# Kernel optimization log

Measured on AMD Instinct MI355X. Metric: run time of the kernel, lower is better.

Reference implementation:

```python
import jax, jax.numpy as jnp
from jax import lax
import numpy as np

HID = 128; NRAD = 32; NAZ = 8; EPS_BN = 1e-5

def _bn(x, p):
    # p: [4, C] = (gamma, beta, running_mean, running_var); eval-mode batchnorm
    g, b, m, v = p
    sh = (1, -1) + (1,) * (x.ndim - 2)
    return (x - m.reshape(sh)) * (g.reshape(sh) / jnp.sqrt(v.reshape(sh) + EPS_BN)) + b.reshape(sh)

def _conv2d(x, w, b):
    y = lax.conv_general_dilated(x, w, (1, 1), 'SAME', dimension_numbers=('NCHW', 'OIHW', 'NCHW'))
    return y + b.reshape(1, -1, 1, 1)

def _conv1d(x, w, b):
    y = lax.conv_general_dilated(x, w, (1,), 'SAME', dimension_numbers=('NCH', 'OIH', 'NCH'))
    return y + b.reshape(1, -1, 1)

def setup_inputs():
    key = jax.random.key(0)
    ks = iter(jax.random.split(key, 48))
    def W(shape, s=0.05):
        return jax.random.normal(next(ks), shape, jnp.float32) * s
    def bias(c):
        return jax.random.normal(next(ks), (c,), jnp.float32) * 0.01
    def bn(c):
        g = 1.0 + 0.1 * jax.random.normal(next(ks), (c,), jnp.float32)
        b = 0.1 * jax.random.normal(next(ks), (c,), jnp.float32)
        m = 0.05 * jax.random.normal(next(ks), (c,), jnp.float32)
        v = 0.5 + jax.random.uniform(next(ks), (c,), jnp.float32)
        return jnp.stack([g, b, m, v])
    B, C, H, Wd = 16, 3, 256, 256
    h2, h4 = HID // 2, HID // 4
    comb = h2 + h4 + h4 + NAZ * C * 2  # 64+32+32+48 = 176
    return {
        'x': jax.random.normal(next(ks), (B, C, H, Wd), jnp.float32),
        'mw1': W((h2, C, 3, 3)), 'mb1': bias(h2), 'mbn1': bn(h2),
        'mw2': W((h2, h2, 3, 3)), 'mb2': bias(h2), 'mbn2': bn(h2),
        'pw1': W((h4, C, 3, 3)), 'pb1': bias(h4), 'pbn1': bn(h4),
        'pw2': W((h4, h4, 3, 3)), 'pb2': bias(h4), 'pbn2': bn(h4),
        'rw1': W((h4, C, 3)), 'rb1': bias(h4), 'rbn1': bn(h4),
        'rw2': W((h4, h4, 3)), 'rb2': bias(h4), 'rbn2': bn(h4),
        'lw1': W((HID * 2, comb)), 'lb1': bias(HID * 2),
        'lng': jnp.ones((HID * 2,), jnp.float32), 'lnb': jnp.zeros((HID * 2,), jnp.float32),
        'lw2': W((HID, HID * 2)), 'lb2': bias(HID),
    }

def _forward(x, mw1, mb1, mbn1, mw2, mb2, mbn2, pw1, pb1, pbn1, pw2, pb2, pbn2,
             rw1, rb1, rbn1, rw2, rb2, rbn2, lw1, lb1, lng, lnb, lw2, lb2):
    B, C, H, Wd = x.shape
    xf = jnp.clip(x.astype(jnp.float32), -10.0, 10.0)
    freq = jnp.fft.rfft2(xf, axes=(-2, -1))                         # [B,C,H,W//2+1] complex
    mag = jnp.clip(jnp.abs(freq), 1e-8, 1e6)
    mag_log = jnp.clip(jnp.log1p(mag), -20.0, 20.0)
    phase = jnp.clip(jnp.angle(freq) / np.pi, -1.0, 1.0)

    # static frequency-grid bin indices
    fy = jnp.fft.fftfreq(H).astype(jnp.float32)
    fx = jnp.fft.rfftfreq(Wd).astype(jnp.float32)
    fyg, fxg = jnp.meshgrid(fy, fx, indexing='ij')
    radius = jnp.sqrt(fxg ** 2 + fyg ** 2)
    rbins = jnp.clip((radius / (radius.max() + 1e-8) * (NRAD - 1)).astype(jnp.int32), 0, NRAD - 1).reshape(-1)
    angle = jnp.arctan2(fyg, fxg + 1e-8)
    abins = jnp.clip(((angle + np.pi) / (2 * np.pi) * NAZ).astype(jnp.int32), 0, NAZ - 1).reshape(-1)

    mag_flat = mag.reshape(B, C, -1)                                # [B,C,N]
    # radial power spectrum: segment mean via one-hot contraction
    r_oh = jax.nn.one_hot(rbins, NRAD, dtype=jnp.float32)           # [N,NRAD]
    r_cnt = jnp.maximum(r_oh.sum(0), 1.0)
    radial = jnp.clip(jnp.einsum('bcn,nk->bck', mag_flat, r_oh) / r_cnt, 0.0, 1e6)  # [B,C,NRAD]

    # azimuthal mean / unbiased std per angular sector (single pass sum/sumsq/count)
    a_oh = jax.nn.one_hot(abins, NAZ, dtype=jnp.float32)            # [N,NAZ]
    a_cnt = a_oh.sum(0)
    s1 = jnp.einsum('bcn,nk->bck', mag_flat, a_oh)
    s2 = jnp.einsum('bcn,nk->bck', mag_flat ** 2, a_oh)
    a_mean = s1 / a_cnt
    a_var = (s2 - a_cnt * a_mean ** 2) / jnp.maximum(a_cnt - 1.0, 1.0)
    a_std = jnp.sqrt(jnp.maximum(a_var, 0.0))
    # torch cat order: mean_bin0, std_bin0, mean_bin1, std_bin1, ... each [B,C]
    az = jnp.stack([a_mean.transpose(0, 2, 1), a_std.transpose(0, 2, 1)], axis=2).reshape(B, NAZ * 2 * C)
    az = jnp.nan_to_num(az, nan=0.0, posinf=1e4, neginf=-1e4)

    # bilinear upsample to (H,W); jax.image.resize uses half-pixel centers == align_corners=False
    mag_sp = jax.image.resize(mag_log, (B, C, H, Wd), 'bilinear')
    ph_sp = jax.image.resize(phase, (B, C, H, Wd), 'bilinear')

    mag_feat = jax.nn.relu(_bn(_conv2d(mag_sp, mw1, mb1), mbn1))
    mag_feat = jax.nn.relu(_bn(_conv2d(mag_feat, mw2, mb2), mbn2))
    mag_pool = mag_feat.mean((2, 3))
    ph_feat = jax.nn.relu(_bn(_conv2d(ph_sp, pw1, pb1), pbn1))
    ph_feat = jax.nn.relu(_bn(_conv2d(ph_feat, pw2, pb2), pbn2))
    ph_pool = ph_feat.mean((2, 3))

    rf = jax.nn.relu(_bn(_conv1d(radial, rw1, rb1), rbn1))
    rf = jax.nn.relu(_bn(_conv1d(rf, rw2, rb2), rbn2))
    rf = rf.mean(-1)                                                # AdaptiveAvgPool1d(1)+Flatten

    comb = jnp.concatenate([mag_pool, ph_pool, rf, az], axis=1)    # [B,176]
    comb = jnp.nan_to_num(comb, nan=0.0, posinf=1e4, neginf=-1e4)
    h = comb @ lw1.T + lb1
    mu = h.mean(-1, keepdims=True)
    var = ((h - mu) ** 2).mean(-1, keepdims=True)
    h = (h - mu) / jnp.sqrt(var + 1e-5) * lng + lnb                 # LayerNorm
    h = jax.nn.relu(h)                                              # dropout = identity (eval)
    out = h @ lw2.T + lb2
    out = jnp.clip(out, -100.0, 100.0)
    return jnp.nan_to_num(out, nan=0.0, posinf=100.0, neginf=-100.0)

def reference(x, mw1, mb1, mbn1, mw2, mb2, mbn2, pw1, pb1, pbn1, pw2, pb2, pbn2,
              rw1, rb1, rbn1, rw2, rb2, rbn2, lw1, lb1, lng, lnb, lw2, lb2):
    return _forward(x, mw1, mb1, mbn1, mw2, mb2, mbn2, pw1, pb1, pbn1, pw2, pb2, pbn2,
                    rw1, rb1, rbn1, rw2, rb2, rbn2, lw1, lb1, lng, lnb, lw2, lb2)
```

## Files before the change

kernel.cpp:

```cpp
#include <hip/hip_runtime.h>
#include <math.h>

#define PI_F 3.14159274101257324f
#define TWO_PI_256 0.02454369260617026f
#define TWO_PI_16  0.39269908169872414f

typedef __attribute__((ext_vector_type(8))) short bf16x8;
typedef __attribute__((ext_vector_type(4))) float f32x4;

static const size_t OFF_FC    = 0;
static const size_t OFF_MLOG  = 3170304;
static const size_t OFF_PH    = 4755456;
static const size_t OFF_RSUM  = 9486336;
static const size_t OFF_RCNT  = OFF_RSUM + 1536;
static const size_t OFF_AS1   = OFF_RCNT + 32;
static const size_t OFF_AS2   = OFF_AS1 + 384;
static const size_t OFF_ACNT  = OFF_AS2 + 384;
static const size_t OFF_MPOOL = OFF_ACNT + 8;
static const size_t OFF_PPOOL = OFF_MPOOL + 1024;
static const size_t OFF_RF    = OFF_PPOOL + 512;
static const size_t OFF_PAR   = OFF_RF + 512;
static const size_t OFF_WBM   = OFF_PAR + 512;
static const size_t OFF_WBP   = OFF_WBM + 18432;
static const size_t OFF_W1BM  = OFF_WBP + 4608;
static const size_t OFF_W1BP  = OFF_W1BM + 1024;

__device__ __forceinline__ float fix_nan(float v, float pinf, float ninf) {
  if (isnan(v)) return 0.f;
  if (isinf(v)) return v > 0.f ? pinf : ninf;
  return v;
}

__device__ __forceinline__ unsigned short f2bf(float f) {
  unsigned u = __float_as_uint(f);
  unsigned r = (u + 0x7FFFu + ((u >> 16) & 1u)) >> 16;
  return (unsigned short)r;
}

__device__ __forceinline__ void fold_bn(const float* bn, int C, int c, float cb,
                                        float* s, float* t) {
  float g = bn[c], b = bn[C + c], m = bn[2 * C + c], v = bn[3 * C + c];
  float sc = g / sqrtf(v + 1e-5f);
  *s = sc;
  *t = b + (cb - m) * sc;
}

__global__ __launch_bounds__(256) void row_fft_prep(
    const float* __restrict__ x, float* __restrict__ Fc, float* __restrict__ zbuf,
    const float* __restrict__ mw1, const float* __restrict__ pw1,
    const float* __restrict__ mw2, const float* __restrict__ pw2,
    const float* __restrict__ mb1, const float* __restrict__ mbn1,
    const float* __restrict__ mb2, const float* __restrict__ mbn2,
    const float* __restrict__ pb1, const float* __restrict__ pbn1,
    const float* __restrict__ pb2, const float* __restrict__ pbn2,
    const float* __restrict__ rb1, const float* __restrict__ rbn1,
    const float* __restrict__ rb2, const float* __restrict__ rbn2,
    float* __restrict__ par, unsigned short* __restrict__ wbm,
    unsigned short* __restrict__ wbp, unsigned short* __restrict__ w1bm,
    unsigned short* __restrict__ w1bp) {
  const int blk = blockIdx.x;
  const int tid = threadIdx.x;
  if (blk >= 12288) {
    int idx = (blk - 12288) * 256 + tid;
    if (idx < 36864) {
      int pos = idx / 4096, rem = idx % 4096;
      int oc = rem >> 6, ci = rem & 63;
      wbm[idx] = f2bf(mw2[(oc * 64 + ci) * 9 + pos]);
    } else if (idx < 46080) {
      int i = idx - 36864;
      int pos = i / 1024, rem = i % 1024;
      int oc = rem >> 5, ci = rem & 31;
      wbp[i] = f2bf(pw2[(oc * 32 + ci) * 9 + pos]);
    } else if (idx < 46336) {
      int i = idx - 46080;
      float s, t;
      if (i < 64)       { fold_bn(mbn1, 64, i, mb1[i], &s, &t);          par[i] = s;       par[64 + i] = t; }
      else if (i < 128) { int c = i - 64;  fold_bn(mbn2, 64, c, mb2[c], &s, &t); par[128 + c] = s; par[192 + c] = t; }
      else if (i < 160) { int c = i - 128; fold_bn(pbn1, 32, c, pb1[c], &s, &t); par[256 + c] = s; par[288 + c] = t; }
      else if (i < 192) { int c = i - 160; fold_bn(pbn2, 32, c, pb2[c], &s, &t); par[320 + c] = s; par[352 + c] = t; }
      else if (i < 224) { int c = i - 192; fold_bn(rbn1, 32, c, rb1[c], &s, &t); par[384 + c] = s; par[416 + c] = t; }
      else              { int c = i - 224; fold_bn(rbn2, 32, c, rb2[c], &s, &t); par[448 + c] = s; par[480 + c] = t; }
    } else if (idx < 48384) {
      int i = idx - 46336;
      int oc = i >> 5, k = i & 31;
      w1bm[i] = (k < 27) ? f2bf(mw1[oc * 27 + k]) : (unsigned short)0;
    } else if (idx < 49408) {
      int i = idx - 48384;
      int oc = i >> 5, k = i & 31;
      w1bp[i] = (k < 27) ? f2bf(pw1[oc * 27 + k]) : (unsigned short)0;
    }
    return;
  }
  if (blk == 0) {
    for (int i = tid; i < 3880; i += 256) zbuf[i] = 0.f;
  }
  __shared__ float xr[256];
  __shared__ float2 sS[256];
  {
    float v = x[(size_t)blk * 256 + tid];
    xr[tid] = fminf(fmaxf(v, -10.f), 10.f);
  }
  __syncthreads();
  {
    int b16 = tid >> 4, m = tid & 15;
    float sW, cW;
    sincosf(TWO_PI_16 * (float)m, &sW, &cW);
    float sr = 0.f, si = 0.f, wr = 1.f, wi = 0.f;
#pragma unroll
    for (int a = 0; a < 16; ++a) {
      float xv = xr[a * 16 + b16];
      sr = fmaf(xv, wr, sr);
      si = fmaf(xv, wi, si);
      float nr = wr * cW + wi * sW;
      float ni = wi * cW - wr * sW;
      wr = nr; wi = ni;
    }
    sS[b16 * 16 + m] = make_float2(sr, si);
  }
  __syncthreads();
  if (tid < 129) {
    int m2 = tid & 15;
    float sK, cK;
    sincosf(TWO_PI_256 * (float)tid, &sK, &cK);
    float fr = 0.f, fi = 0.f, wr = 1.f, wi = 0.f;
#pragma unroll
    for (int bb = 0; bb < 16; ++bb) {
      float2 s = sS[bb * 16 + m2];
      fr = fmaf(s.x, wr, fr); fr = fmaf(-s.y, wi, fr);
      fi = fmaf(s.x, wi, fi); fi = fmaf(s.y, wr, fi);
      float nr = wr * cK + wi * sK;
      float ni = wi * cK - wr * sK;
      wr = nr; wi = ni;
    }
    float2* o = (float2*)Fc;
    o[(size_t)blk * 129 + tid] = make_float2(fr, fi);
  }
}

__global__ __launch_bounds__(256) void col_fft_stats(
    const float* __restrict__ Fc, float* __restrict__ mlog, float* __restrict__ ph,
    float* __restrict__ rsum, float* __restrict__ rcnt, float* __restrict__ as1,
    float* __restrict__ as2, float* __restrict__ acnt) {
  const int k = blockIdx.x, b = blockIdx.y;
  const int tid = threadIdx.x;
  const int cp = tid >> 7;
  __shared__ float2 col[3][256];
  __shared__ float2 sS[3][256];
  __shared__ float l_rs[3][2][32];
  __shared__ float l_rc[32];
  __shared__ float l_s1[3][2][8], l_s2[3][2][8];
  __shared__ float l_ac[8];
  for (int i = tid; i < 192; i += 256) {
    int c = i / 64, r = i % 64;
    l_rs[c][r >> 5][r & 31] = 0.f;
  }
  if (tid < 32) l_rc[tid] = 0.f;
  if (tid < 48) { int c = tid / 16, r = tid % 16; l_s1[c][r >> 3][r & 7] = 0.f; l_s2[c][r >> 3][r & 7] = 0.f; }
  if (tid < 8) l_ac[tid] = 0.f;
  const float2* fc = (const float2*)Fc;
#pragma unroll
  for (int c = 0; c < 3; ++c)
    col[c][tid] = fc[((size_t)((b * 3 + c) * 256) + tid) * 129 + k];
  __syncthreads();
  {
    int b16 = tid >> 4, m = tid & 15;
    float sW, cW;
    sincosf(TWO_PI_16 * (float)m, &sW, &cW);
#pragma unroll
    for (int c = 0; c < 3; ++c) {
      float sr = 0.f, si = 0.f, wr = 1.f, wi = 0.f;
#pragma unroll
      for (int a = 0; a < 16; ++a) {
        float2 v = col[c][a * 16 + b16];
        sr = fmaf(v.x, wr, sr); sr = fmaf(-v.y, wi, sr);
        si = fmaf(v.x, wi, si); si = fmaf(v.y, wr, si);
        float nr = wr * cW + wi * sW;
        float ni = wi * cW - wr * sW;
        wr = nr; wi = ni;
      }
      sS[c][b16 * 16 + m] = make_float2(sr, si);
    }
  }
  __syncthreads();
  const int j = tid;
  float sK, cK;
  sincosf(TWO_PI_256 * (float)j, &sK, &cK);
  float gr[3], gi[3];
#pragma unroll
  for (int c = 0; c < 3; ++c) {
    float fr = 0.f, fi = 0.f, wr = 1.f, wi = 0.f;
#pragma unroll
    for (int bb = 0; bb < 16; ++bb) {
      float2 s = sS[c][bb * 16 + (j & 15)];
      fr = fmaf(s.x, wr, fr); fr = fmaf(-s.y, wi, fr);
      fi = fmaf(s.x, wi, fi); fi = fmaf(s.y, wr, fi);
      float nr = wr * cK + wi * sK;
      float ni = wi * cK - wr * sK;
      wr = nr; wi = ni;
    }
    gr[c] = fr; gi[c] = fi;
  }
  float fy = (float)(j < 128 ? j : j - 256) * (1.0f / 256.0f);
  float fx = (float)k * (1.0f / 256.0f);
  float rad = sqrtf(fx * fx + fy * fy);
  float denom = sqrtf(0.5f) + 1e-8f;
  int rb = (int)((rad / denom) * 31.0f);
  rb = rb < 0 ? 0 : (rb > 31 ? 31 : rb);
  float ang = atan2f(fy, fx + 1e-8f);
  int ab = (int)((ang + PI_F) / (2.0f * PI_F) * 8.0f);
  ab = ab < 0 ? 0 : (ab > 7 ? 7 : ab);
#pragma unroll
  for (int c = 0; c < 3; ++c) {
    float mag = sqrtf(gr[c] * gr[c] + gi[c] * gi[c]);
    mag = fminf(fmaxf(mag, 1e-8f), 1e6f);
    float ml = fminf(fmaxf(log1pf(mag), -20.f), 20.f);
    float p = fminf(fmaxf(atan2f(gi[c], gr[c]) / PI_F, -1.f), 1.f);
    size_t oidx = ((size_t)((b * 3 + c) * 256) + j) * 129 + k;
    mlog[oidx] = ml;
    ph[oidx] = p;
    atomicAdd(&l_rs[c][cp][rb], mag);
    atomicAdd(&l_s1[c][cp][ab], mag);
    atomicAdd(&l_s2[c][cp][ab], mag * mag);
  }
  if (b == 0) {
    atomicAdd(&l_rc[rb], 1.0f);
    atomicAdd(&l_ac[ab], 1.0f);
  }
  __syncthreads();
  if (tid < 96) {
    int c = tid / 32, i2 = tid % 32;
    atomicAdd(&rsum[(b * 3 + c) * 32 + i2], l_rs[c][0][i2] + l_rs[c][1][i2]);
  } else if (tid < 120) {
    int t2 = tid - 96;
    int c = t2 / 8, a2 = t2 % 8;
    atomicAdd(&as1[(b * 3 + c) * 8 + a2], l_s1[c][0][a2] + l_s1[c][1][a2]);
    atomicAdd(&as2[(b * 3 + c) * 8 + a2], l_s2[c][0][a2] + l_s2[c][1][a2]);
  }
  if (b == 0) {
    if (tid < 32) atomicAdd(&rcnt[tid], l_rc[tid]);
    else if (tid < 40) atomicAdd(&acnt[tid - 32], l_ac[tid - 32]);
  }
}

template <int C2>
__global__ __launch_bounds__(256, (C2 == 64 ? 3 : 4)) void conv_mfma(
    const float* __restrict__ src,
    const unsigned short* __restrict__ w1b,
    const unsigned short* __restrict__ wB,
    const float* __restrict__ s1, const float* __restrict__ t1,
    const float* __restrict__ s2, const float* __restrict__ t2,
    float* __restrict__ pool) {
  constexpr int HALVES = C2 / 32;
  constexpr int ST = 40;
  constexpr int WNT = C2 / 32;

  __shared__ float s_in[3][20][20];
  __shared__ float s_sc1[C2], s_sh1[C2];
  __shared__ __align__(16) unsigned short s_f1[324 * ST];

  const int tid = threadIdx.x;
  const int b = blockIdx.z;
  const int tx0 = blockIdx.x * 16, ty0 = blockIdx.y * 16;
  const int lane = tid & 63, wv = tid >> 6;
  const int ln = lane & 15, q = lane >> 4;
  const int ntg = wv & 1, half_w = wv >> 1;
  const int ocb0 = ntg * WNT * 16;

  for (int idx = tid; idx < 1200; idx += 256) {
    int c = idx / 400, r = idx % 400, iy = r / 20, ix = r % 20;
    int gy = ty0 - 2 + iy, gx = tx0 - 2 + ix;
    float v = 0.f;
    if ((unsigned)gy < 256u && (unsigned)gx < 256u) {
      float srcx = ((float)gx + 0.5f) * (129.0f / 256.0f) - 0.5f;
      float fl = floorf(srcx);
      float w = srcx - fl;
      int x0 = (int)fl, x1 = x0 + 1;
      x0 = x0 < 0 ? 0 : x0;
      x1 = x1 > 128 ? 128 : x1;
      const float* rowp = src + ((size_t)(b * 3 + c) * 256 + gy) * 129;
      v = rowp[x0] * (1.f - w) + rowp[x1] * w;
    }
    s_in[c][iy][ix] = v;
  }
  if (tid < C2) { s_sc1[tid] = s1[tid]; s_sh1[tid] = t1[tid]; }
  __syncthreads();

  const float* sp = &s_in[0][0][0];
  int koff[8];
#pragma unroll
  for (int j = 0; j < 8; ++j) {
    int k = q * 8 + j;
    if (k < 27) {
      int c = k / 9, rr = k - c * 9, dy = rr / 3, dx = rr - dy * 3;
      koff[j] = (c * 20 + dy) * 20 + dx;
    } else koff[j] = -1;
  }

  f32x4 acc[WNT][8];
#pragma unroll
  for (int w = 0; w < WNT; ++w)
#pragma unroll
    for (int i = 0; i < 8; ++i)
      acc[w][i] = (f32x4){0.f, 0.f, 0.f, 0.f};

  const int rbase = half_w * 8;

  for (int hf = 0; hf < HALVES; ++hf) {
    if (hf > 0) __syncthreads();
    bf16x8 b1h[2];
    float c1sc[2][4], c1sh[2][4];
#pragma unroll
    for (int w = 0; w < 2; ++w) {
      int nt = hf * 2 + w;
      b1h[w] = *(const bf16x8*)&w1b[(nt * 16 + ln) * 32 + q * 8];
#pragma unroll
      for (int r = 0; r < 4; ++r) {
        c1sc[w][r] = s_sc1[hf * 32 + w * 16 + q * 4 + r];
        c1sh[w][r] = s_sh1[hf * 32 + w * 16 + q * 4 + r];
      }
    }
    for (int mt = wv; mt < 21; mt += 4) {
      int p = mt * 16 + ln;
      int pc = p < 324 ? p : 0;
      int py = pc / 18, px = pc - py * 18;
      int pix = py * 20 + px;
      union { bf16x8 v; unsigned u[4]; } af;
#pragma unroll
      for (int jj = 0; jj < 4; ++jj) {
        float v0 = (koff[2 * jj] >= 0) ? sp[koff[2 * jj] + pix] : 0.f;
        float v1 = (koff[2 * jj + 1] >= 0) ? sp[koff[2 * jj + 1] + pix] : 0.f;
        af.u[jj] = (unsigned)f2bf(v0) | ((unsigned)f2bf(v1) << 16);
      }
      bool inim = false;
      if (p < 324) {
        int gy = ty0 - 1 + py, gx = tx0 - 1 + px;
        inim = ((unsigned)gy < 256u) && ((unsigned)gx < 256u);
      }
#pragma unroll
      for (int w = 0; w < 2; ++w) {
        f32x4 c1 = __builtin_amdgcn_mfma_f32_16x16x32_bf16(
            b1h[w], af.v, (f32x4){0.f, 0.f, 0.f, 0.f}, 0, 0, 0);
        if (p < 324) {
          float v0 = inim ? fmaxf(fmaf(c1[0], c1sc[w][0], c1sh[w][0]), 0.f) : 0.f;
          float v1 = inim ? fmaxf(fmaf(c1[1], c1sc[w][1], c1sh[w][1]), 0.f) : 0.f;
          float v2 = inim ? fmaxf(fmaf(c1[2], c1sc[w][2], c1sh[w][2]), 0.f) : 0.f;
          float v3 = inim ? fmaxf(fmaf(c1[3], c1sc[w][3], c1sh[w][3]), 0.f) : 0.f;
          uint2 pk;
          pk.x = (unsigned)f2bf(v0) | ((unsigned)f2bf(v1) << 16);
          pk.y = (unsigned)f2bf(v2) | ((unsigned)f2bf(v3) << 16);
          *(uint2*)&s_f1[p * ST + w * 16 + q * 4] = pk;
        }
      }
    }
    __syncthreads();
#pragma unroll
    for (int kx = 0; kx < 3; ++kx) {
      bf16x8 Bf[WNT * 3];
#pragma unroll
      for (int w = 0; w < WNT; ++w)
#pragma unroll
        for (int ky = 0; ky < 3; ++ky)
          Bf[w * 3 + ky] = *(const bf16x8*)&wB[((size_t)(ky * 3 + kx) * C2 + ocb0 + w * 16 + ln) * C2 +
                                               hf * 32 + q * 8];
      bf16x8 a[10];
#pragma unroll
      for (int rr = 0; rr < 10; ++rr)
        a[rr] = *(const bf16x8*)&s_f1[((rbase + rr) * 18 + ln + kx) * ST + q * 8];
#pragma unroll
      for (int ky = 0; ky < 3; ++ky)
#pragma unroll
        for (int w = 0; w < WNT; ++w)
#pragma unroll
          for (int i = 0; i < 8; ++i)
            acc[w][i] = __builtin_amdgcn_mfma_f32_16x16x32_bf16(a[i + ky], Bf[w * 3 + ky],
                                                                acc[w][i], 0, 0, 0);
    }
  }

#pragma unroll
  for (int w = 0; w < WNT; ++w) {
    const int oc = ocb0 + w * 16 + ln;
    const float sc = s2[oc], sh = t2[oc];
    float v = 0.f;
#pragma unroll
    for (int i = 0; i < 8; ++i)
#pragma unroll
      for (int r = 0; r < 4; ++r)
        v += fmaxf(fmaf(acc[w][i][r], sc, sh), 0.f);
    v += __shfl_xor(v, 16);
    v += __shfl_xor(v, 32);
    if (q == 0) atomicAdd(&pool[b * C2 + oc], v);
  }
}

__global__ __launch_bounds__(256) void final_mlp(
    const float* __restrict__ rsum, const float* __restrict__ rcnt,
    const float* __restrict__ rw1, const float* __restrict__ rw2,
    const float* __restrict__ sr1, const float* __restrict__ tr1,
    const float* __restrict__ sr2, const float* __restrict__ tr2,
    const float* __restrict__ mpool, const float* __restrict__ ppool,
    const float* __restrict__ as1, const float* __restrict__ as2,
    const float* __restrict__ acnt,
    const float* __restrict__ lw1, const float* __restrict__ lb1,
    const float* __restrict__ lng, const float* __restrict__ lnb,
    const float* __restrict__ lw2, const float* __restrict__ lb2,
    float* __restrict__ out) {
  int b = blockIdx.x, t = threadIdx.x;
  __shared__ float rad[3][32];
  __shared__ float rf1[32][32];
  __shared__ float rf2[32][32];
  __shared__ float rfv[32];
  __shared__ float comb[176];
  __shared__ float red[256];
  __shared__ float hrelu[256];
  __shared__ float s_mu, s_var;

  if (t < 96) {
    int c = t / 32, i = t % 32;
    float cnt = fmaxf(rcnt[i], 1.0f);
    float v = rsum[(b * 3 + c) * 32 + i] / cnt;
    rad[c][i] = fminf(fmaxf(v, 0.f), 1e6f);
  }
  __syncthreads();
  for (int idx = t; idx < 1024; idx += 256) {
    int oc = idx >> 5, i = idx & 31;
    float a = 0.f;
    for (int c = 0; c < 3; ++c)
#pragma unroll
      for (int d = 0; d < 3; ++d) {
        int ii = i + d - 1;
        if (ii >= 0 && ii < 32) a = fmaf(rad[c][ii], rw1[(oc * 3 + c) * 3 + d], a);
      }
    rf1[oc][i] = fmaxf(fmaf(a, sr1[oc], tr1[oc]), 0.f);
  }
  __syncthreads();
  for (int idx = t; idx < 1024; idx += 256) {
    int oc = idx >> 5, i = idx & 31;
    float a = 0.f;
    for (int c = 0; c < 32; ++c)
#pragma unroll
      for (int d = 0; d < 3; ++d) {
        int ii = i + d - 1;
        if (ii >= 0 && ii < 32) a = fmaf(rf1[c][ii], rw2[(oc * 32 + c) * 3 + d], a);
      }
    rf2[oc][i] = fmaxf(fmaf(a, sr2[oc], tr2[oc]), 0.f);
  }
  __syncthreads();
  if (t < 32) {
    float s = 0.f;
    for (int i = 0; i < 32; ++i) s += rf2[t][i];
    rfv[t] = s * (1.0f / 32.0f);
  }
  __syncthreads();

  if (t < 64) comb[t] = fix_nan(mpool[b * 64 + t] * (1.0f / 65536.0f), 1e4f, -1e4f);
  else if (t < 96) comb[t] = fix_nan(ppool[b * 32 + t - 64] * (1.0f / 65536.0f), 1e4f, -1e4f);
  else if (t < 128) comb[t] = fix_nan(rfv[t - 96], 1e4f, -1e4f);
  else if (t < 176) {
    int j = t - 128;
    int a = j / 6, r = j % 6, m = r / 3, c = r % 3;
    float cnt = acnt[a];
    float v = 0.f;
    if (cnt > 0.f) {
      float s1v = as1[(b * 3 + c) * 8 + a], s2v = as2[(b * 3 + c) * 8 + a];
      float mean = s1v / cnt;
      if (m == 0)
        v = mean;
      else {
        float var = (s2v - cnt * mean * mean) / fmaxf(cnt - 1.f, 1.f);
        v = sqrtf(fmaxf(var, 0.f));
      }
    }
    comb[t] = fix_nan(v, 1e4f, -1e4f);
  }
  __syncthreads();
  float h = lb1[t];
  const float* wr = lw1 + t * 176;
#pragma unroll 8
  for (int j = 0; j < 176; ++j) h = fmaf(comb[j], wr[j], h);
  red[t] = h;
  __syncthreads();
  for (int s = 128; s > 0; s >>= 1) {
    if (t < s) red[t] += red[t + s];
    __syncthreads();
  }
  if (t == 0) s_mu = red[0] * (1.0f / 256.0f);
  __syncthreads();
  float mu = s_mu;
  float d = h - mu;
  red[t] = d * d;
  __syncthreads();
  for (int s = 128; s > 0; s >>= 1) {
    if (t < s) red[t] += red[t + s];
    __syncthreads();
  }
  if (t == 0) s_var = red[0] * (1.0f / 256.0f);
  __syncthreads();
  float hn = d / sqrtf(s_var + 1e-5f) * lng[t] + lnb[t];
  hrelu[t] = fmaxf(hn, 0.f);
  __syncthreads();
  if (t < 128) {
    float o = lb2[t];
    const float* w2r = lw2 + t * 256;
#pragma unroll 8
    for (int j = 0; j < 256; ++j) o = fmaf(hrelu[j], w2r[j], o);
    o = fminf(fmaxf(o, -100.f), 100.f);
    out[b * 128 + t] = fix_nan(o, 100.f, -100.f);
  }
}

extern "C" void kernel_launch(void* const* d_in, const int* in_sizes, int n_in,
                              void* d_out, int out_size, void* d_ws, size_t ws_size,
                              hipStream_t stream) {
  const float* x    = (const float*)d_in[0];
  const float* mw1  = (const float*)d_in[1];
  const float* mb1  = (const float*)d_in[2];
  const float* mbn1 = (const float*)d_in[3];
  const float* mw2  = (const float*)d_in[4];
  const float* mb2  = (const float*)d_in[5];
  const float* mbn2 = (const float*)d_in[6];
  const float* pw1  = (const float*)d_in[7];
  const float* pb1  = (const float*)d_in[8];
  const float* pbn1 = (const float*)d_in[9];
  const float* pw2  = (const float*)d_in[10];
  const float* pb2  = (const float*)d_in[11];
  const float* pbn2 = (const float*)d_in[12];
  const float* rw1  = (const float*)d_in[13];
  const float* rb1  = (const float*)d_in[14];
  const float* rbn1 = (const float*)d_in[15];
  const float* rw2  = (const float*)d_in[16];
  const float* rb2  = (const float*)d_in[17];
  const float* rbn2 = (const float*)d_in[18];
  const float* lw1  = (const float*)d_in[19];
  const float* lb1  = (const float*)d_in[20];
  const float* lng  = (const float*)d_in[21];
  const float* lnb  = (const float*)d_in[22];
  const float* lw2  = (const float*)d_in[23];
  const float* lb2  = (const float*)d_in[24];

  float* ws = (float*)d_ws;
  float* out = (float*)d_out;

  float* fc    = ws + OFF_FC;
  float* mlog  = ws + OFF_MLOG;
  float* phb   = ws + OFF_PH;
  float* rsum  = ws + OFF_RSUM;
  float* rcnt  = ws + OFF_RCNT;
  float* as1   = ws + OFF_AS1;
  float* as2   = ws + OFF_AS2;
  float* acnt  = ws + OFF_ACNT;
  float* mpool = ws + OFF_MPOOL;
  float* ppool = ws + OFF_PPOOL;
  float* par   = ws + OFF_PAR;
  unsigned short* wbm  = (unsigned short*)(ws + OFF_WBM);
  unsigned short* wbp  = (unsigned short*)(ws + OFF_WBP);
  unsigned short* w1bm = (unsigned short*)(ws + OFF_W1BM);
  unsigned short* w1bp = (unsigned short*)(ws + OFF_W1BP);

  row_fft_prep<<<12481, 256, 0, stream>>>(x, fc, rsum,
                                          mw1, pw1, mw2, pw2, mb1, mbn1, mb2, mbn2,
                                          pb1, pbn1, pb2, pbn2, rb1, rbn1, rb2, rbn2,
                                          par, wbm, wbp, w1bm, w1bp);
  col_fft_stats<<<dim3(129, 16), 256, 0, stream>>>(fc, mlog, phb, rsum, rcnt,
                                                   as1, as2, acnt);
  conv_mfma<64><<<dim3(16, 16, 16), 256, 0, stream>>>(
      mlog, w1bm, wbm, par + 0, par + 64, par + 128, par + 192, mpool);
  conv_mfma<32><<<dim3(16, 16, 16), 256, 0, stream>>>(
      phb, w1bp, wbp, par + 256, par + 288, par + 320, par + 352, ppool);
  final_mlp<<<16, 256, 0, stream>>>(rsum, rcnt, rw1, rw2, par + 384, par + 416,
                                    par + 448, par + 480, mpool, ppool, as1, as2,
                                    acnt, lw1, lb1, lng, lnb, lw2, lb2, out);
}
```

Before: 460.1 us.

## Merge magnitude and phase convs into one launch, prefetch weights, transpose spectrum layout

Combines the two conv_mfma launches into a single conv_both kernel whose z-dimension picks the magnitude (64-channel) or phase (32-channel) path. This removes one launch and lets the two workloads share the GPU at the same time. Weight fragments for the next (half, kx) step are double-buffered in registers so the global loads overlap the MFMA work. The log-magnitude and phase buffers now use a [k][j] layout, which changes write coalescing in the FFT-stats kernel and read patterns in the conv gather. The trade-offs are higher register pressure on the 32-channel path and occupancy tied to the 64-channel launch bound.

```diff
diff --git a/kernel.cpp b/kernel.cpp
--- a/kernel.cpp
+++ b/kernel.cpp
@@ -215,7 +215,7 @@
     mag = fminf(fmaxf(mag, 1e-8f), 1e6f);
     float ml = fminf(fmaxf(log1pf(mag), -20.f), 20.f);
     float p = fminf(fmaxf(atan2f(gi[c], gr[c]) / PI_F, -1.f), 1.f);
-    size_t oidx = ((size_t)((b * 3 + c) * 256) + j) * 129 + k;
+    size_t oidx = ((size_t)((b * 3 + c) * 129) + k) * 256 + j;
     mlog[oidx] = ml;
     ph[oidx] = p;
     atomicAdd(&l_rs[c][cp][rb], mag);
@@ -243,24 +243,19 @@
 }
 
 template <int C2>
-__global__ __launch_bounds__(256, (C2 == 64 ? 3 : 4)) void conv_mfma(
+__device__ __forceinline__ void conv_impl(
     const float* __restrict__ src,
     const unsigned short* __restrict__ w1b,
     const unsigned short* __restrict__ wB,
     const float* __restrict__ s1, const float* __restrict__ t1,
     const float* __restrict__ s2, const float* __restrict__ t2,
-    float* __restrict__ pool) {
+    float* __restrict__ pool, int b, int tx0, int ty0, int tid,
+    float (&s_in)[3][20][20], float* s_sc1, float* s_sh1, unsigned short* s_f1) {
   constexpr int HALVES = C2 / 32;
   constexpr int ST = 40;
   constexpr int WNT = C2 / 32;
-
-  __shared__ float s_in[3][20][20];
-  __shared__ float s_sc1[C2], s_sh1[C2];
-  __shared__ __align__(16) unsigned short s_f1[324 * ST];
-
-  const int tid = threadIdx.x;
-  const int b = blockIdx.z;
-  const int tx0 = blockIdx.x * 16, ty0 = blockIdx.y * 16;
+  constexpr int G = HALVES * 3;
+
   const int lane = tid & 63, wv = tid >> 6;
   const int ln = lane & 15, q = lane >> 4;
   const int ntg = wv & 1, half_w = wv >> 1;
@@ -277,12 +272,21 @@
       int x0 = (int)fl, x1 = x0 + 1;
       x0 = x0 < 0 ? 0 : x0;
       x1 = x1 > 128 ? 128 : x1;
-      const float* rowp = src + ((size_t)(b * 3 + c) * 256 + gy) * 129;
-      v = rowp[x0] * (1.f - w) + rowp[x1] * w;
+      const float* cp = src + (size_t)(b * 3 + c) * (129 * 256);
+      v = cp[x0 * 256 + gy] * (1.f - w) + cp[x1 * 256 + gy] * w;
     }
     s_in[c][iy][ix] = v;
   }
   if (tid < C2) { s_sc1[tid] = s1[tid]; s_sh1[tid] = t1[tid]; }
+
+  bf16x8 Bb[2][WNT * 3];
+#pragma unroll
+  for (int w = 0; w < WNT; ++w)
+#pragma unroll
+    for (int ky = 0; ky < 3; ++ky)
+      Bb[0][w * 3 + ky] =
+          *(const bf16x8*)&wB[((size_t)(ky * 3 + 0) * C2 + ocb0 + w * 16 + ln) * C2 + 0 + q * 8];
+
   __syncthreads();
 
   const float* sp = &s_in[0][0][0];
@@ -305,6 +309,7 @@
 
   const int rbase = half_w * 8;
 
+#pragma unroll
   for (int hf = 0; hf < HALVES; ++hf) {
     if (hf > 0) __syncthreads();
     bf16x8 b1h[2];
@@ -355,13 +360,17 @@
     __syncthreads();
 #pragma unroll
     for (int kx = 0; kx < 3; ++kx) {
-      bf16x8 Bf[WNT * 3];
-#pragma unroll
-      for (int w = 0; w < WNT; ++w)
-#pragma unroll
-        for (int ky = 0; ky < 3; ++ky)
-          Bf[w * 3 + ky] = *(const bf16x8*)&wB[((size_t)(ky * 3 + kx) * C2 + ocb0 + w * 16 + ln) * C2 +
-                                               hf * 32 + q * 8];
+      const int g = hf * 3 + kx;
+      if (g + 1 < G) {
+        const int nhf = (g + 1) / 3, nkx = (g + 1) % 3;
+#pragma unroll
+        for (int w = 0; w < WNT; ++w)
+#pragma unroll
+          for (int ky = 0; ky < 3; ++ky)
+            Bb[(g + 1) & 1][w * 3 + ky] =
+                *(const bf16x8*)&wB[((size_t)(ky * 3 + nkx) * C2 + ocb0 + w * 16 + ln) * C2 +
+                                    nhf * 32 + q * 8];
+      }
       bf16x8 a[10];
 #pragma unroll
       for (int rr = 0; rr < 10; ++rr)
@@ -372,7 +381,7 @@
         for (int w = 0; w < WNT; ++w)
 #pragma unroll
           for (int i = 0; i < 8; ++i)
-            acc[w][i] = __builtin_amdgcn_mfma_f32_16x16x32_bf16(a[i + ky], Bf[w * 3 + ky],
+            acc[w][i] = __builtin_amdgcn_mfma_f32_16x16x32_bf16(a[i + ky], Bb[g & 1][w * 3 + ky],
                                                                 acc[w][i], 0, 0, 0);
     }
   }
@@ -391,6 +400,25 @@
     v += __shfl_xor(v, 32);
     if (q == 0) atomicAdd(&pool[b * C2 + oc], v);
   }
+}
+
+__global__ __launch_bounds__(256, 3) void conv_both(
+    const float* __restrict__ msrc, const float* __restrict__ psrc,
+    const unsigned short* __restrict__ w1bm, const unsigned short* __restrict__ w1bp,
+    const unsigned short* __restrict__ wbm, const unsigned short* __restrict__ wbp,
+    const float* __restrict__ par, float* __restrict__ mpool, float* __restrict__ ppool) {
+  __shared__ float s_in[3][20][20];
+  __shared__ float s_sc1[64], s_sh1[64];
+  __shared__ __align__(16) unsigned short s_f1[324 * 40];
+  const int tid = threadIdx.x;
+  const int tx0 = blockIdx.x * 16, ty0 = blockIdx.y * 16;
+  const int z = blockIdx.z;
+  if (z < 16)
+    conv_impl<64>(msrc, w1bm, wbm, par + 0, par + 64, par + 128, par + 192,
+                  mpool, z, tx0, ty0, tid, s_in, s_sc1, s_sh1, s_f1);
+  else
+    conv_impl<32>(psrc, w1bp, wbp, par + 256, par + 288, par + 320, par + 352,
+                  ppool, z - 16, tx0, ty0, tid, s_in, s_sc1, s_sh1, s_f1);
 }
 
 __global__ __launch_bounds__(256) void final_mlp(
@@ -563,10 +591,8 @@
                                           par, wbm, wbp, w1bm, w1bp);
   col_fft_stats<<<dim3(129, 16), 256, 0, stream>>>(fc, mlog, phb, rsum, rcnt,
                                                    as1, as2, acnt);
-  conv_mfma<64><<<dim3(16, 16, 16), 256, 0, stream>>>(
-      mlog, w1bm, wbm, par + 0, par + 64, par + 128, par + 192, mpool);
-  conv_mfma<32><<<dim3(16, 16, 16), 256, 0, stream>>>(
-      phb, w1bp, wbp, par + 256, par + 288, par + 320, par + 352, ppool);
+  conv_both<<<dim3(16, 16, 32), 256, 0, stream>>>(mlog, phb, w1bm, w1bp, wbm, wbp,
+                                                  par, mpool, ppool);
   final_mlp<<<16, 256, 0, stream>>>(rsum, rcnt, rw1, rw2, par + 384, par + 416,
                                     par + 448, par + 480, mpool, ppool, as1, as2,
                                     acnt, lw1, lb1, lng, lnb, lw2, lb2, out);
```

Result: slower. 549.7 us (+19.5%).

## Compute full conv1 tile once and double-buffer conv2 weight loads

Applied to the files above, without the earlier changes.

Conv1 output for all channels is now computed once into a wider shared tile instead of in 32-channel halves, which removes the extra barrier and per-half recompute. Conv2 weights are prefetched before the first barrier. For the 64-channel case they are double-buffered in registers across the kx/k-slice loop, and for the 32-channel case they stay fully resident. The change also lowers launch bounds to 2 blocks per SM and enlarges shared memory per block, so occupancy may drop in exchange for fewer syncs and better load overlap.

```diff
diff --git a/kernel.cpp b/kernel.cpp
--- a/kernel.cpp
+++ b/kernel.cpp
@@ -243,16 +243,18 @@
 }
 
 template <int C2>
-__global__ __launch_bounds__(256, (C2 == 64 ? 3 : 4)) void conv_mfma(
+__global__ __launch_bounds__(256, 2) void conv_mfma(
     const float* __restrict__ src,
     const unsigned short* __restrict__ w1b,
     const unsigned short* __restrict__ wB,
     const float* __restrict__ s1, const float* __restrict__ t1,
     const float* __restrict__ s2, const float* __restrict__ t2,
     float* __restrict__ pool) {
-  constexpr int HALVES = C2 / 32;
-  constexpr int ST = 40;
-  constexpr int WNT = C2 / 32;
+  constexpr int ST = C2 + 8;
+  constexpr int NT = C2 / 16;
+  constexpr int WNT = (C2 == 64) ? 2 : 1;
+  constexpr int KS = C2 / 32;
+  constexpr int NG = 3 * KS;
 
   __shared__ float s_in[3][20][20];
   __shared__ float s_sc1[C2], s_sh1[C2];
@@ -263,7 +265,7 @@
   const int tx0 = blockIdx.x * 16, ty0 = blockIdx.y * 16;
   const int lane = tid & 63, wv = tid >> 6;
   const int ln = lane & 15, q = lane >> 4;
-  const int ntg = wv & 1, half_w = wv >> 1;
+  const int ntg = wv & 1, half = wv >> 1;
   const int ocb0 = ntg * WNT * 16;
 
   for (int idx = tid; idx < 1200; idx += 256) {
@@ -283,7 +285,40 @@
     s_in[c][iy][ix] = v;
   }
   if (tid < C2) { s_sc1[tid] = s1[tid]; s_sh1[tid] = t1[tid]; }
-  __syncthreads();
+
+  bf16x8 b1[NT];
+#pragma unroll
+  for (int nt = 0; nt < NT; ++nt)
+    b1[nt] = *(const bf16x8*)&w1b[(nt * 16 + ln) * 32 + q * 8];
+
+  bf16x8 Bb[2][3 * WNT];
+  bf16x8 Bw[(C2 == 32) ? 9 : 1];
+  if constexpr (C2 == 64) {
+#pragma unroll
+    for (int ky = 0; ky < 3; ++ky)
+#pragma unroll
+      for (int w = 0; w < 2; ++w)
+        Bb[0][ky * 2 + w] =
+            *(const bf16x8*)&wB[((size_t)(ky * 3) * 64 + ocb0 + w * 16 + ln) * 64 + q * 8];
+  } else {
+#pragma unroll
+    for (int kx = 0; kx < 3; ++kx)
+#pragma unroll
+      for (int ky = 0; ky < 3; ++ky)
+        Bw[kx * 3 + ky] =
+            *(const bf16x8*)&wB[((size_t)(ky * 3 + kx) * 32 + ocb0 + ln) * 32 + q * 8];
+  }
+
+  __syncthreads();
+
+  float c1sc[NT][4], c1sh[NT][4];
+#pragma unroll
+  for (int nt = 0; nt < NT; ++nt)
+#pragma unroll
+    for (int r = 0; r < 4; ++r) {
+      c1sc[nt][r] = s_sc1[nt * 16 + q * 4 + r];
+      c1sh[nt][r] = s_sh1[nt * 16 + q * 4 + r];
+    }
 
   const float* sp = &s_in[0][0][0];
   int koff[8];
@@ -295,6 +330,40 @@
       koff[j] = (c * 20 + dy) * 20 + dx;
     } else koff[j] = -1;
   }
+  for (int mt = wv; mt < 21; mt += 4) {
+    int p = mt * 16 + ln;
+    int pc = p < 324 ? p : 0;
+    int py = pc / 18, px = pc - py * 18;
+    int pix = py * 20 + px;
+    union { bf16x8 v; unsigned u[4]; } af;
+#pragma unroll
+    for (int jj = 0; jj < 4; ++jj) {
+      float v0 = (koff[2 * jj] >= 0) ? sp[koff[2 * jj] + pix] : 0.f;
+      float v1 = (koff[2 * jj + 1] >= 0) ? sp[koff[2 * jj + 1] + pix] : 0.f;
+      af.u[jj] = (unsigned)f2bf(v0) | ((unsigned)f2bf(v1) << 16);
+    }
+    bool inim = false;
+    if (p < 324) {
+      int gy = ty0 - 1 + py, gx = tx0 - 1 + px;
+      inim = ((unsigned)gy < 256u) && ((unsigned)gx < 256u);
+    }
+#pragma unroll
+    for (int nt = 0; nt < NT; ++nt) {
+      f32x4 c1 = __builtin_amdgcn_mfma_f32_16x16x32_bf16(
+          b1[nt], af.v, (f32x4){0.f, 0.f, 0.f, 0.f}, 0, 0, 0);
+      if (p < 324) {
+        float v0 = inim ? fmaxf(fmaf(c1[0], c1sc[nt][0], c1sh[nt][0]), 0.f) : 0.f;
+        float v1 = inim ? fmaxf(fmaf(c1[1], c1sc[nt][1], c1sh[nt][1]), 0.f) : 0.f;
+        float v2 = inim ? fmaxf(fmaf(c1[2], c1sc[nt][2], c1sh[nt][2]), 0.f) : 0.f;
+        float v3 = inim ? fmaxf(fmaf(c1[3], c1sc[nt][3], c1sh[nt][3]), 0.f) : 0.f;
+        uint2 pk;
+        pk.x = (unsigned)f2bf(v0) | ((unsigned)f2bf(v1) << 16);
+        pk.y = (unsigned)f2bf(v2) | ((unsigned)f2bf(v3) << 16);
+        *(uint2*)&s_f1[p * ST + nt * 16 + q * 4] = pk;
+      }
+    }
+  }
+  __syncthreads();
 
   f32x4 acc[WNT][8];
 #pragma unroll
@@ -303,78 +372,37 @@
     for (int i = 0; i < 8; ++i)
       acc[w][i] = (f32x4){0.f, 0.f, 0.f, 0.f};
 
-  const int rbase = half_w * 8;
-
-  for (int hf = 0; hf < HALVES; ++hf) {
-    if (hf > 0) __syncthreads();
-    bf16x8 b1h[2];
-    float c1sc[2][4], c1sh[2][4];
-#pragma unroll
-    for (int w = 0; w < 2; ++w) {
-      int nt = hf * 2 + w;
-      b1h[w] = *(const bf16x8*)&w1b[(nt * 16 + ln) * 32 + q * 8];
-#pragma unroll
-      for (int r = 0; r < 4; ++r) {
-        c1sc[w][r] = s_sc1[hf * 32 + w * 16 + q * 4 + r];
-        c1sh[w][r] = s_sh1[hf * 32 + w * 16 + q * 4 + r];
+  const int rbase = half * 8;
+#pragma unroll
+  for (int g = 0; g < NG; ++g) {
+    const int kx = g / KS, ks = g % KS;
+    if constexpr (C2 == 64) {
+      if (g + 1 < NG) {
+        const int nkx = (g + 1) / KS, nks = (g + 1) % KS;
+#pragma unroll
+        for (int ky = 0; ky < 3; ++ky)
+#pragma unroll
+          for (int w = 0; w < 2; ++w)
+            Bb[(g + 1) & 1][ky * 2 + w] =
+                *(const bf16x8*)&wB[((size_t)(ky * 3 + nkx) * 64 + ocb0 + w * 16 + ln) * 64 +
+                                    nks * 32 + q * 8];
       }
     }
-    for (int mt = wv; mt < 21; mt += 4) {
-      int p = mt * 16 + ln;
-      int pc = p < 324 ? p : 0;
-      int py = pc / 18, px = pc - py * 18;
-      int pix = py * 20 + px;
-      union { bf16x8 v; unsigned u[4]; } af;
-#pragma unroll
-      for (int jj = 0; jj < 4; ++jj) {
-        float v0 = (koff[2 * jj] >= 0) ? sp[koff[2 * jj] + pix] : 0.f;
-        float v1 = (koff[2 * jj + 1] >= 0) ? sp[koff[2 * jj + 1] + pix] : 0.f;
-        af.u[jj] = (unsigned)f2bf(v0) | ((unsigned)f2bf(v1) << 16);
+    bf16x8 a[10];
+#pragma unroll
+    for (int rr = 0; rr < 10; ++rr)
+      a[rr] = *(const bf16x8*)&s_f1[((rbase + rr) * 18 + ln + kx) * ST + ks * 32 + q * 8];
+#pragma unroll
+    for (int ky = 0; ky < 3; ++ky)
+#pragma unroll
+      for (int w = 0; w < WNT; ++w) {
+        bf16x8 bf;
+        if constexpr (C2 == 64) bf = Bb[g & 1][ky * 2 + w];
+        else bf = Bw[kx * 3 + ky];
+#pragma unroll
+        for (int i = 0; i < 8; ++i)
+          acc[w][i] = __builtin_amdgcn_mfma_f32_16x16x32_bf16(a[i + ky], bf, acc[w][i], 0, 0, 0);
       }
-      bool inim = false;
-      if (p < 324) {
-        int gy = ty0 - 1 + py, gx = tx0 - 1 + px;
-        inim = ((unsigned)gy < 256u) && ((unsigned)gx < 256u);
-      }
-#pragma unroll
-      for (int w = 0; w < 2; ++w) {
-        f32x4 c1 = __builtin_amdgcn_mfma_f32_16x16x32_bf16(
-            b1h[w], af.v, (f32x4){0.f, 0.f, 0.f, 0.f}, 0, 0, 0);
-        if (p < 324) {
-          float v0 = inim ? fmaxf(fmaf(c1[0], c1sc[w][0], c1sh[w][0]), 0.f) : 0.f;
-          float v1 = inim ? fmaxf(fmaf(c1[1], c1sc[w][1], c1sh[w][1]), 0.f) : 0.f;
-          float v2 = inim ? fmaxf(fmaf(c1[2], c1sc[w][2], c1sh[w][2]), 0.f) : 0.f;
-          float v3 = inim ? fmaxf(fmaf(c1[3], c1sc[w][3], c1sh[w][3]), 0.f) : 0.f;
-          uint2 pk;
-          pk.x = (unsigned)f2bf(v0) | ((unsigned)f2bf(v1) << 16);
-          pk.y = (unsigned)f2bf(v2) | ((unsigned)f2bf(v3) << 16);
-          *(uint2*)&s_f1[p * ST + w * 16 + q * 4] = pk;
-        }
-      }
-    }
-    __syncthreads();
-#pragma unroll
-    for (int kx = 0; kx < 3; ++kx) {
-      bf16x8 Bf[WNT * 3];
-#pragma unroll
-      for (int w = 0; w < WNT; ++w)
-#pragma unroll
-        for (int ky = 0; ky < 3; ++ky)
-          Bf[w * 3 + ky] = *(const bf16x8*)&wB[((size_t)(ky * 3 + kx) * C2 + ocb0 + w * 16 + ln) * C2 +
-                                               hf * 32 + q * 8];
-      bf16x8 a[10];
-#pragma unroll
-      for (int rr = 0; rr < 10; ++rr)
-        a[rr] = *(const bf16x8*)&s_f1[((rbase + rr) * 18 + ln + kx) * ST + q * 8];
-#pragma unroll
-      for (int ky = 0; ky < 3; ++ky)
-#pragma unroll
-        for (int w = 0; w < WNT; ++w)
-#pragma unroll
-          for (int i = 0; i < 8; ++i)
-            acc[w][i] = __builtin_amdgcn_mfma_f32_16x16x32_bf16(a[i + ky], Bf[w * 3 + ky],
-                                                                acc[w][i], 0, 0, 0);
-    }
   }
 
 #pragma unroll
```

Result: faster. 443.2 us (-3.7%).
